# Kernel tuning notes

Measured on AMD Instinct MI355X. Metric: run time of the kernel, lower is better.

## Reference

```python
import jax, jax.numpy as jnp
import numpy as np

B, S, E, H = 2, 2048, 1024, 16
D = E // H  # head_dim = 64
FE = 4      # forward_expansion
EPS = 1e-5


def layernorm(x, g, b):
    mu = jnp.mean(x, axis=-1, keepdims=True)
    var = jnp.var(x, axis=-1, keepdims=True)
    return (x - mu) * jax.lax.rsqrt(var + EPS) * g + b


def setup_inputs() -> dict:
    key = jax.random.key(0)
    ks = jax.random.split(key, 16)
    s = lambda d: 1.0 / np.sqrt(d)
    return {
        "queries": jax.random.normal(ks[0], (B, S, E), jnp.float32),
        "keys": jax.random.normal(ks[1], (B, S, E), jnp.float32),
        "values": jax.random.normal(ks[2], (B, S, E), jnp.float32),
        "mask": jnp.ones((B, 1, S, S), jnp.int32),  # ignored (faithful to source bug)
        "Wq": jax.random.normal(ks[3], (D, D), jnp.float32) * s(D),
        "Wk": jax.random.normal(ks[4], (D, D), jnp.float32) * s(D),
        "Wv": jax.random.normal(ks[5], (D, D), jnp.float32) * s(D),
        "Wfc": jax.random.normal(ks[6], (E, E), jnp.float32) * s(E),
        "bfc": jnp.zeros((E,), jnp.float32),
        "W1": jax.random.normal(ks[7], (FE * E, E), jnp.float32) * s(E),
        "b1": jnp.zeros((FE * E,), jnp.float32),
        "W2": jax.random.normal(ks[8], (E, FE * E), jnp.float32) * s(FE * E),
        "b2": jnp.zeros((E,), jnp.float32),
        "ln1_g": jnp.ones((E,), jnp.float32),
        "ln1_b": jnp.zeros((E,), jnp.float32),
        "ln2_g": jnp.ones((E,), jnp.float32),
        "ln2_b": jnp.zeros((E,), jnp.float32),
    }


def reference(queries, keys, values, mask, Wq, Wk, Wv, Wfc, bfc, W1, b1, W2, b2,
              ln1_g, ln1_b, ln2_g, ln2_b):
    # --- MHA ---
    q = queries.reshape(B, S, H, D) @ Wq.T  # [B,S,H,D]
    k = keys.reshape(B, S, H, D) @ Wk.T
    v = values.reshape(B, S, H, D) @ Wv.T
    scores = jnp.einsum('bqhd,bkhd->bhqk', q, k)
    # source: softmax(scores / S**(-1/2)) == scores * sqrt(S)  (faithful quirk)
    # mask is ignored: source masked_fill is non-inplace and discarded
    attn = jax.nn.softmax(scores * jnp.sqrt(jnp.float32(S)), axis=-1)
    out = jnp.einsum('bhqk,bkhd->bqhd', attn, v).reshape(B, S, E)
    att = out @ Wfc.T + bfc
    # --- residual + LN + FFN + LN (dropout p=0 -> identity) ---
    h = layernorm(att + queries, ln1_g, ln1_b)
    x = jax.nn.relu(h @ W1.T + b1) @ W2.T + b2
    return layernorm(x + h, ln2_g, ln2_b)
```

## Files before the change

### kernel.cpp

```cpp
#include <hip/hip_runtime.h>
#include <hip/hip_bf16.h>
#include <math.h>

#define B_ 2
#define S_ 2048
#define E_ 1024
#define H_ 16
#define D_ 64
#define TOK (B_*S_)
#define SCALE2 (45.254833995939045f * 1.44269504088896340f)

typedef __bf16 bf16x8 __attribute__((ext_vector_type(8)));
typedef float floatx4 __attribute__((ext_vector_type(4)));
struct b4s { __hip_bfloat16 x, y, z, w; };

typedef const __attribute__((address_space(1))) char ga_char;
typedef __attribute__((address_space(3))) char ls_char;

__device__ __forceinline__ void gload_lds16(const void* g, ls_char* l) {
  __builtin_amdgcn_global_load_lds((ga_char*)g, l, 16, 0, 0);
}

#if __has_builtin(__builtin_amdgcn_exp2f)
#define EXP2(x) __builtin_amdgcn_exp2f(x)
#else
#define EXP2(x) exp2f(x)
#endif

#define SWZ(arr, half, row, qpos) \
  (*(bf16x8*)&arr[half][row][(((qpos) ^ ((row) & 3)) * 8)])

__device__ __forceinline__ void sbar() {
  asm volatile("" ::: "memory");
  __builtin_amdgcn_s_barrier();
  asm volatile("" ::: "memory");
}

__global__ __launch_bounds__(256) void cast_all(
    const float* __restrict__ Wfc, const float* __restrict__ W1,
    const float* __restrict__ W2, __hip_bfloat16* __restrict__ Wfcb,
    __hip_bfloat16* __restrict__ W1b, __hip_bfloat16* __restrict__ W2b,
    const float* __restrict__ Wq, const float* __restrict__ Wk,
    const float* __restrict__ Wv, __hip_bfloat16* __restrict__ Whl) {
  const int i = blockIdx.x * 256 + threadIdx.x;
  if (i < 2359296) {
    const float* src; __hip_bfloat16* dst; int j;
    if (i < 262144)       { src = Wfc; dst = Wfcb; j = i; }
    else if (i < 1310720) { src = W1;  dst = W1b;  j = i - 262144; }
    else                  { src = W2;  dst = W2b;  j = i - 1310720; }
    float4 v = ((const float4*)src)[j];
    b4s o;
    o.x = __float2bfloat16(v.x); o.y = __float2bfloat16(v.y);
    o.z = __float2bfloat16(v.z); o.w = __float2bfloat16(v.w);
    *(b4s*)(dst + (size_t)j * 4) = o;
  } else if (i < 2362368) {
    const int idx = i - 2359296;
    const int m = idx >> 10;
    const int off = (idx & 1023) * 4;
    const float* W = (m == 0) ? Wq : (m == 1) ? Wk : Wv;
    float4 v = *(const float4*)(W + off);
    b4s hi, lo;
    hi.x = __float2bfloat16(v.x); lo.x = __float2bfloat16(v.x - __bfloat162float(hi.x));
    hi.y = __float2bfloat16(v.y); lo.y = __float2bfloat16(v.y - __bfloat162float(hi.y));
    hi.z = __float2bfloat16(v.z); lo.z = __float2bfloat16(v.z - __bfloat162float(hi.z));
    hi.w = __float2bfloat16(v.w); lo.w = __float2bfloat16(v.w - __bfloat162float(hi.w));
    *(b4s*)(Whl + (size_t)m * 8192 + off) = hi;
    *(b4s*)(Whl + (size_t)m * 8192 + 4096 + off) = lo;
  }
}

__global__ __launch_bounds__(256) void qkv_fused(
    const float* __restrict__ xq, const float* __restrict__ xk,
    const float* __restrict__ xv, const __hip_bfloat16* __restrict__ Whl,
    __hip_bfloat16* __restrict__ qhi, __hip_bfloat16* __restrict__ qlo,
    __hip_bfloat16* __restrict__ khi, __hip_bfloat16* __restrict__ klo,
    __hip_bfloat16* __restrict__ vt) {
  __shared__ __bf16 Xh[2][64][32], Xl[2][64][32];
  __shared__ __bf16 Vt[64][72];
  const int t = threadIdx.x, lane = t & 63, w = t >> 6;
  const int quad = lane >> 4, low = lane & 15;
  const int bh = blockIdx.y;
  const int b = bh >> 4, h = bh & 15;
  const int s0 = blockIdx.x * 64;
  const int sr = t >> 2;
  const int sc = (t & 3) * 16;
  const int scc = sc >> 5;
  const int p0 = (sc & 31) >> 3;

  for (int m = 0; m < 3; m++) {
    const float* xin = (m == 0) ? xq : (m == 1) ? xk : xv;
    const __hip_bfloat16* Wh = Whl + (size_t)m * 8192;
    const float sc_m = (m == 0) ? SCALE2 : 1.0f;

    __syncthreads();
    {
      const float* src = xin + ((size_t)(b * S_ + s0 + sr)) * E_ + h * 64 + sc;
      float4 f0 = *(const float4*)(src);
      float4 f1 = *(const float4*)(src + 4);
      float4 f2 = *(const float4*)(src + 8);
      float4 f3 = *(const float4*)(src + 12);
      float fv[16] = {f0.x, f0.y, f0.z, f0.w, f1.x, f1.y, f1.z, f1.w,
                      f2.x, f2.y, f2.z, f2.w, f3.x, f3.y, f3.z, f3.w};
      bf16x8 hi0, hi1, lo0, lo1;
      #pragma unroll
      for (int j = 0; j < 8; j++) {
        hi0[j] = (__bf16)fv[j];
        lo0[j] = (__bf16)(fv[j] - (float)hi0[j]);
        hi1[j] = (__bf16)fv[8 + j];
        lo1[j] = (__bf16)(fv[8 + j] - (float)hi1[j]);
      }
      SWZ(Xh, scc, sr, p0) = hi0;
      SWZ(Xh, scc, sr, p0 + 1) = hi1;
      SWZ(Xl, scc, sr, p0) = lo0;
      SWZ(Xl, scc, sr, p0 + 1) = lo1;
    }
    __syncthreads();

    bf16x8 ah[2], al[2];
    #pragma unroll
    for (int c = 0; c < 2; c++) {
      ah[c] = SWZ(Xh, c, w * 16 + low, quad);
      al[c] = SWZ(Xl, c, w * 16 + low, quad);
    }

    floatx4 acc[4];
    #pragma unroll
    for (int nn = 0; nn < 4; nn++) {
      floatx4 a = {};
      #pragma unroll
      for (int c = 0; c < 2; c++) {
        const __hip_bfloat16* wp = Wh + (nn * 16 + low) * 64 + c * 32 + quad * 8;
        bf16x8 wh_ = *(const bf16x8*)wp;
        bf16x8 wl_ = *(const bf16x8*)(wp + 4096);
        a = __builtin_amdgcn_mfma_f32_16x16x32_bf16(ah[c], wh_, a, 0, 0, 0);
        a = __builtin_amdgcn_mfma_f32_16x16x32_bf16(al[c], wh_, a, 0, 0, 0);
        a = __builtin_amdgcn_mfma_f32_16x16x32_bf16(ah[c], wl_, a, 0, 0, 0);
      }
      acc[nn] = a;
    }

    if (m < 2) {
      __hip_bfloat16* dh = (m == 0) ? qhi : khi;
      __hip_bfloat16* dl = (m == 0) ? qlo : klo;
      #pragma unroll
      for (int nn = 0; nn < 4; nn++) {
        #pragma unroll
        for (int i = 0; i < 4; i++) {
          const int s = s0 + w * 16 + quad * 4 + i;
          const int d = nn * 16 + low;
          const size_t adr = ((size_t)bh * S_ + s) * 64 + d;
          const float f = acc[nn][i] * sc_m;
          const __hip_bfloat16 hb = __float2bfloat16(f);
          dh[adr] = hb;
          dl[adr] = __float2bfloat16(f - __bfloat162float(hb));
        }
      }
    } else {
      #pragma unroll
      for (int nn = 0; nn < 4; nn++)
        #pragma unroll
        for (int i = 0; i < 4; i++)
          Vt[nn * 16 + low][w * 16 + quad * 4 + i] = (__bf16)acc[nn][i];
      __syncthreads();
      const int dr = t >> 2;
      const int scl = (t & 3) * 16;
      __hip_bfloat16* dst = vt + ((size_t)bh * 64 + dr) * S_ + s0 + scl;
      bf16x8 o0 = *(const bf16x8*)&Vt[dr][scl];
      bf16x8 o1 = *(const bf16x8*)&Vt[dr][scl + 8];
      *(bf16x8*)dst = o0;
      *(bf16x8*)(dst + 8) = o1;
    }
  }
}

__device__ __forceinline__ void softmax_update(
    const floatx4* sa, floatx4* oacc, float& mrow, float& lrow, bf16x8* pb) {
  float rmax;
  {
    float m0 = fmaxf(fmaxf(sa[0][0], sa[0][1]), fmaxf(sa[0][2], sa[0][3]));
    float m1 = fmaxf(fmaxf(sa[1][0], sa[1][1]), fmaxf(sa[1][2], sa[1][3]));
    float m2 = fmaxf(fmaxf(sa[2][0], sa[2][1]), fmaxf(sa[2][2], sa[2][3]));
    float m3 = fmaxf(fmaxf(sa[3][0], sa[3][1]), fmaxf(sa[3][2], sa[3][3]));
    rmax = fmaxf(fmaxf(m0, m1), fmaxf(m2, m3));
    rmax = fmaxf(rmax, __shfl_xor(rmax, 16, 64));
    rmax = fmaxf(rmax, __shfl_xor(rmax, 32, 64));
  }
  if (__any(rmax > mrow)) {
    const float nm = fmaxf(mrow, rmax);
    const float al = EXP2(mrow - nm);
    mrow = nm;
    lrow *= al;
    #pragma unroll
    for (int dt = 0; dt < 4; dt++) {
      oacc[dt][0] *= al; oacc[dt][1] *= al;
      oacc[dt][2] *= al; oacc[dt][3] *= al;
    }
  }
  float p[4][4];
  float rs;
  {
    float r0_ = 0.f, r1_ = 0.f, r2_ = 0.f, r3_ = 0.f;
    #pragma unroll
    for (int i = 0; i < 4; i++) {
      p[0][i] = EXP2(sa[0][i] - mrow); r0_ += p[0][i];
      p[1][i] = EXP2(sa[1][i] - mrow); r1_ += p[1][i];
      p[2][i] = EXP2(sa[2][i] - mrow); r2_ += p[2][i];
      p[3][i] = EXP2(sa[3][i] - mrow); r3_ += p[3][i];
    }
    rs = (r0_ + r1_) + (r2_ + r3_);
    rs += __shfl_xor(rs, 16, 64);
    rs += __shfl_xor(rs, 32, 64);
  }
  lrow += rs;
  #pragma unroll
  for (int kh2 = 0; kh2 < 2; kh2++) {
    bf16x8 v;
    v[0] = (__bf16)p[kh2][0]; v[1] = (__bf16)p[kh2][1];
    v[2] = (__bf16)p[kh2][2]; v[3] = (__bf16)p[kh2][3];
    v[4] = (__bf16)p[kh2 + 2][0]; v[5] = (__bf16)p[kh2 + 2][1];
    v[6] = (__bf16)p[kh2 + 2][2]; v[7] = (__bf16)p[kh2 + 2][3];
    pb[kh2] = v;
  }
}

__global__ __launch_bounds__(512, 4) void attn_mfma(
    const __hip_bfloat16* __restrict__ Qhi, const __hip_bfloat16* __restrict__ Qlo,
    const __hip_bfloat16* __restrict__ Khi, const __hip_bfloat16* __restrict__ Klo,
    const __hip_bfloat16* __restrict__ Vtg, __hip_bfloat16* __restrict__ ctx) {
  __shared__ __bf16 Kh[2][2][64][32], Kl[2][2][64][32], Vs[2][2][64][32];
  const int t = threadIdx.x, lane = t & 63, w = t >> 6;
  const int quad = lane >> 4, low = lane & 15;
  const int bh = blockIdx.x;
  const int qw = blockIdx.y * 128 + w * 16;

  const int sh = w >> 2;
  const int r0 = (w & 3) * 16;
  const int srow = r0 + (lane >> 2);
  const int sq = (lane & 3) ^ (srow & 3);
  const __hip_bfloat16* gK = Khi + ((size_t)bh * S_ + srow) * 64 + sh * 32 + sq * 8;
  const __hip_bfloat16* gL = Klo + ((size_t)bh * S_ + srow) * 64 + sh * 32 + sq * 8;
  const __hip_bfloat16* gV = Vtg + ((size_t)bh * 64 + srow) * S_ + sh * 32 + sq * 8;

  bf16x8 qh[2], ql[2];
  {
    const size_t qbase = ((size_t)bh * S_ + qw + low) * 64 + quad * 8;
    qh[0] = *(const bf16x8*)(Qhi + qbase);
    qh[1] = *(const bf16x8*)(Qhi + qbase + 32);
    ql[0] = *(const bf16x8*)(Qlo + qbase);
    ql[1] = *(const bf16x8*)(Qlo + qbase + 32);
  }

  floatx4 oacc[4] = {};
  float mrow = -3e38f, lrow = 0.f;

  gload_lds16(gK, (ls_char*)&Kh[0][sh][r0][0]);
  gload_lds16(gL, (ls_char*)&Kl[0][sh][r0][0]);
  gload_lds16(gV, (ls_char*)&Vs[0][sh][r0][0]);

  for (int kt = 0; kt < S_ / 64; kt++) {
    const int cur = kt & 1;
    __syncthreads();
    if (kt + 1 < S_ / 64) {
      gload_lds16(gK + (size_t)(kt + 1) * 4096, (ls_char*)&Kh[cur ^ 1][sh][r0][0]);
      gload_lds16(gL + (size_t)(kt + 1) * 4096, (ls_char*)&Kl[cur ^ 1][sh][r0][0]);
      gload_lds16(gV + (size_t)(kt + 1) * 64,   (ls_char*)&Vs[cur ^ 1][sh][r0][0]);
    }

    floatx4 sa[4];
    __builtin_amdgcn_s_setprio(1);
    #pragma unroll
    for (int nn = 0; nn < 4; nn++) {
      const int prow = (nn & 1) * 32 + (nn >> 1) * 4 + (low >> 2) * 8 + (low & 3);
      bf16x8 kh0 = SWZ(Kh[cur], 0, prow, quad);
      bf16x8 kh1 = SWZ(Kh[cur], 1, prow, quad);
      bf16x8 kl0 = SWZ(Kl[cur], 0, prow, quad);
      bf16x8 kl1 = SWZ(Kl[cur], 1, prow, quad);
      floatx4 s = {};
      s = __builtin_amdgcn_mfma_f32_16x16x32_bf16(kh0, qh[0], s, 0, 0, 0);
      s = __builtin_amdgcn_mfma_f32_16x16x32_bf16(kh1, qh[1], s, 0, 0, 0);
      s = __builtin_amdgcn_mfma_f32_16x16x32_bf16(kl0, qh[0], s, 0, 0, 0);
      s = __builtin_amdgcn_mfma_f32_16x16x32_bf16(kl1, qh[1], s, 0, 0, 0);
      s = __builtin_amdgcn_mfma_f32_16x16x32_bf16(kh0, ql[0], s, 0, 0, 0);
      s = __builtin_amdgcn_mfma_f32_16x16x32_bf16(kh1, ql[1], s, 0, 0, 0);
      sa[nn] = s;
    }
    __builtin_amdgcn_s_setprio(0);

    bf16x8 pb[2];
    softmax_update(sa, oacc, mrow, lrow, pb);

    __builtin_amdgcn_s_setprio(1);
    #pragma unroll
    for (int dt = 0; dt < 4; dt++) {
      bf16x8 vb0 = SWZ(Vs[cur], 0, dt * 16 + low, quad);
      bf16x8 vb1 = SWZ(Vs[cur], 1, dt * 16 + low, quad);
      oacc[dt] = __builtin_amdgcn_mfma_f32_16x16x32_bf16(vb0, pb[0], oacc[dt], 0, 0, 0);
      oacc[dt] = __builtin_amdgcn_mfma_f32_16x16x32_bf16(vb1, pb[1], oacc[dt], 0, 0, 0);
    }
    __builtin_amdgcn_s_setprio(0);
  }

  const float inv = 1.0f / lrow;
  const int b = bh >> 4, h = bh & 15;
  const size_t base = ((size_t)(b * S_ + qw + low)) * E_ + h * 64 + quad * 4;
  #pragma unroll
  for (int dt = 0; dt < 4; dt++) {
    b4s o;
    o.x = __float2bfloat16(oacc[dt][0] * inv);
    o.y = __float2bfloat16(oacc[dt][1] * inv);
    o.z = __float2bfloat16(oacc[dt][2] * inv);
    o.w = __float2bfloat16(oacc[dt][3] * inv);
    *(b4s*)(ctx + base + dt * 16) = o;
  }
}

template <int RELU, int OUT_BF16, int PARTIAL>
__global__ __launch_bounds__(256) void gemm_mfma(
    const __hip_bfloat16* __restrict__ A, const __hip_bfloat16* __restrict__ Wt,
    const float* __restrict__ bias, void* __restrict__ C0, void* __restrict__ C1,
    int M, int N, int Kblk, int lda) {
  __shared__ __bf16 As[2][128][64];
  __shared__ __bf16 Bs[2][128][64];
  const int t = threadIdx.x;
  const int lane = t & 63;
  const int w = t >> 6;
  const int wr = w >> 1, wc = w & 1;
  const int m0 = blockIdx.y * 128, n0 = blockIdx.x * 128;
  void* Cout = (blockIdx.z == 0) ? C0 : C1;

  A += (size_t)blockIdx.z * Kblk;
  Wt += (size_t)blockIdx.z * Kblk;

  floatx4 acc[4][4] = {};
  const int srow = t >> 3;
  const int ssc = ((t & 7) ^ (srow & 7)) * 8;

  const __hip_bfloat16* gA = A + (size_t)(m0 + srow) * lda + ssc;
  const __hip_bfloat16* gB = Wt + (size_t)(n0 + srow) * lda + ssc;
  const size_t rstep = (size_t)32 * lda;

#define GSTAGE(buf, k0) do {                                      \
    ls_char* lA = (ls_char*)&As[buf][0][0] + w * 1024;            \
    ls_char* lB = (ls_char*)&Bs[buf][0][0] + w * 1024;            \
    gload_lds16(gA + (k0),             lA);                       \
    gload_lds16(gA + (k0) + rstep,     lA + 4096);                \
    gload_lds16(gA + (k0) + 2 * rstep, lA + 8192);                \
    gload_lds16(gA + (k0) + 3 * rstep, lA + 12288);               \
    gload_lds16(gB + (k0),             lB);                       \
    gload_lds16(gB + (k0) + rstep,     lB + 4096);                \
    gload_lds16(gB + (k0) + 2 * rstep, lB + 8192);                \
    gload_lds16(gB + (k0) + 3 * rstep, lB + 12288);               \
  } while (0)

  GSTAGE(0, 0);
  const int nsteps = Kblk >> 6;
  for (int st = 0; st < nsteps; st++) {
    const int cur = st & 1;
    __syncthreads();
    if (st + 1 < nsteps) GSTAGE(cur ^ 1, (st + 1) * 64);

    #pragma unroll
    for (int ks = 0; ks < 2; ks++) {
      bf16x8 af[4], bfr[4];
      #pragma unroll
      for (int i = 0; i < 4; i++) {
        const int ra = wr * 64 + i * 16 + (lane & 15);
        const int ca = (((lane >> 4) + ks * 4) ^ (ra & 7)) * 8;
        af[i] = *(const bf16x8*)&As[cur][ra][ca];
        const int rb = wc * 64 + i * 16 + (lane & 15);
        const int cb = (((lane >> 4) + ks * 4) ^ (rb & 7)) * 8;
        bfr[i] = *(const bf16x8*)&Bs[cur][rb][cb];
      }
      #pragma unroll
      for (int mi = 0; mi < 4; mi++)
        #pragma unroll
        for (int ni = 0; ni < 4; ni++)
          acc[mi][ni] = __builtin_amdgcn_mfma_f32_16x16x32_bf16(
              af[mi], bfr[ni], acc[mi][ni], 0, 0, 0);
    }
  }
#undef GSTAGE

  const int cil = lane & 15;
  const int quad = lane >> 4;
  #pragma unroll
  for (int ni = 0; ni < 4; ni++) {
    const int col = n0 + wc * 64 + ni * 16 + cil;
    const float bb = PARTIAL ? 0.f : bias[col];
    #pragma unroll
    for (int mi = 0; mi < 4; mi++) {
      const int row = m0 + wr * 64 + mi * 16 + quad * 4;
      #pragma unroll
      for (int i = 0; i < 4; i++) {
        if (PARTIAL) {
          ((float*)Cout)[(size_t)(row + i) * N + col] = acc[mi][ni][i];
        } else {
          float vv = acc[mi][ni][i] + bb;
          if (RELU) vv = fmaxf(vv, 0.f);
          if (OUT_BF16)
            ((__hip_bfloat16*)Cout)[(size_t)(row + i) * N + col] = __float2bfloat16(vv);
          else
            ((float*)Cout)[(size_t)(row + i) * N + col] = vv;
        }
      }
    }
  }
}

__global__ __launch_bounds__(512, 2) void gemm_ff1(
    const __hip_bfloat16* __restrict__ A, const __hip_bfloat16* __restrict__ Wt,
    const float* __restrict__ bias, __hip_bfloat16* __restrict__ C) {
  __shared__ __bf16 As[2][256][64];
  __shared__ __bf16 Bs[2][256][64];
  const int t = threadIdx.x, lane = t & 63, w = t >> 6;
  const int quad = lane >> 4, low = lane & 15;
  const int wm = w >> 2, wn = w & 3;
  const int m0 = blockIdx.y * 256, n0 = blockIdx.x * 256;

  floatx4 acc[8][4] = {};

  const int srow = t >> 3;
  const int ssc = ((t & 7) ^ (srow & 7)) * 8;
  const __hip_bfloat16* gA = A + (size_t)(m0 + srow) * 1024 + ssc;
  const __hip_bfloat16* gB = Wt + (size_t)(n0 + srow) * 1024 + ssc;

#define FSTAGE(buf, k0) do {                                        \
    ls_char* lA = (ls_char*)&As[buf][0][0] + w * 1024;              \
    ls_char* lB = (ls_char*)&Bs[buf][0][0] + w * 1024;              \
    gload_lds16(gA + (k0),          lA);                            \
    gload_lds16(gA + (k0) + 65536,  lA + 8192);                     \
    gload_lds16(gA + (k0) + 131072, lA + 16384);                    \
    gload_lds16(gA + (k0) + 196608, lA + 24576);                    \
    gload_lds16(gB + (k0),          lB);                            \
    gload_lds16(gB + (k0) + 65536,  lB + 8192);                     \
    gload_lds16(gB + (k0) + 131072, lB + 16384);                    \
    gload_lds16(gB + (k0) + 196608, lB + 24576);                    \
  } while (0)

#define LDA_HALF(mh) do {                                                     \
    _Pragma("unroll")                                                         \
    for (int mi = 0; mi < 4; mi++) {                                          \
      const int ra = wm * 128 + (mh) * 64 + mi * 16 + low;                    \
      af[mi][0] = *(const bf16x8*)&As[cur][ra][((quad) ^ (ra & 7)) * 8];      \
      af[mi][1] = *(const bf16x8*)&As[cur][ra][((4 + quad) ^ (ra & 7)) * 8];  \
    }                                                                         \
  } while (0)

#define LDB_HALF(dst, nh) do {                                                \
    _Pragma("unroll")                                                         \
    for (int ni = 0; ni < 2; ni++) {                                          \
      const int rb = wn * 64 + (nh) * 32 + ni * 16 + low;                     \
      dst[ni][0] = *(const bf16x8*)&Bs[cur][rb][((quad) ^ (rb & 7)) * 8];     \
      dst[ni][1] = *(const bf16x8*)&Bs[cur][rb][((4 + quad) ^ (rb & 7)) * 8]; \
    }                                                                         \
  } while (0)

#define MFMA_Q(bfr, mh, nh) do {                                              \
    __builtin_amdgcn_s_setprio(1);                                            \
    _Pragma("unroll")                                                         \
    for (int mi = 0; mi < 4; mi++)                                            \
      _Pragma("unroll")                                                       \
      for (int ni = 0; ni < 2; ni++) {                                        \
        acc[(mh)*4+mi][(nh)*2+ni] = __builtin_amdgcn_mfma_f32_16x16x32_bf16(  \
            af[mi][0], bfr[ni][0], acc[(mh)*4+mi][(nh)*2+ni], 0, 0, 0);       \
        acc[(mh)*4+mi][(nh)*2+ni] = __builtin_amdgcn_mfma_f32_16x16x32_bf16(  \
            af[mi][1], bfr[ni][1], acc[(mh)*4+mi][(nh)*2+ni], 0, 0, 0);       \
      }                                                                       \
    __builtin_amdgcn_s_setprio(0);                                            \
  } while (0)

  FSTAGE(0, 0);
  bf16x8 af[4][2], bA[2][2], bB[2][2];

  for (int kt = 0; kt < 16; kt++) {
    const int cur = kt & 1;
    __syncthreads();

    LDA_HALF(0);
    LDB_HALF(bA, 0);
    sbar();
    MFMA_Q(bA, 0, 0);
    sbar();

    LDB_HALF(bB, 1);
    if (kt + 1 < 16) FSTAGE(cur ^ 1, (kt + 1) * 64);
    sbar();
    MFMA_Q(bB, 0, 1);
    sbar();

    LDA_HALF(1);
    sbar();
    MFMA_Q(bB, 1, 1);
    sbar();

    MFMA_Q(bA, 1, 0);
  }
#undef FSTAGE
#undef LDA_HALF
#undef LDB_HALF
#undef MFMA_Q

  #pragma unroll
  for (int ni = 0; ni < 4; ni++) {
    const int col = n0 + wn * 64 + ni * 16 + low;
    const float bb = bias[col];
    #pragma unroll
    for (int mi = 0; mi < 8; mi++) {
      const int row = m0 + wm * 128 + mi * 16 + quad * 4;
      #pragma unroll
      for (int i = 0; i < 4; i++) {
        float vv = fmaxf(acc[mi][ni][i] + bb, 0.f);
        C[(size_t)(row + i) * 4096 + col] = __float2bfloat16(vv);
      }
    }
  }
}

template <int EMIT_BF16, int HAS_A1, int HAS_BIAS>
__global__ __launch_bounds__(256) void add_ln(
    const float* __restrict__ a0, const float* __restrict__ a1,
    const float* __restrict__ r, const float* __restrict__ bias,
    const float* __restrict__ g, const float* __restrict__ bt,
    float* __restrict__ out, __hip_bfloat16* __restrict__ outb) {
  __shared__ float red[16];
  const int tok = blockIdx.x, t = threadIdx.x;
  float4 av = ((const float4*)(a0 + (size_t)tok * E_))[t];
  float4 rv = ((const float4*)(r + (size_t)tok * E_))[t];
  float4 x;
  x.x = av.x + rv.x; x.y = av.y + rv.y; x.z = av.z + rv.z; x.w = av.w + rv.w;
  if (HAS_A1) {
    float4 a2 = ((const float4*)(a1 + (size_t)tok * E_))[t];
    x.x += a2.x; x.y += a2.y; x.z += a2.z; x.w += a2.w;
  }
  if (HAS_BIAS) {
    float4 cv = ((const float4*)bias)[t];
    x.x += cv.x; x.y += cv.y; x.z += cv.z; x.w += cv.w;
  }
  float sum = x.x + x.y + x.z + x.w;
  float ssq = x.x * x.x + x.y * x.y + x.z * x.z + x.w * x.w;
  #pragma unroll
  for (int off = 32; off >= 1; off >>= 1) {
    sum += __shfl_down(sum, off, 64);
    ssq += __shfl_down(ssq, off, 64);
  }
  const int wave = t >> 6;
  if ((t & 63) == 0) { red[wave] = sum; red[4 + wave] = ssq; }
  __syncthreads();
  if (t == 0) {
    float s = red[0] + red[1] + red[2] + red[3];
    float qq = red[4] + red[5] + red[6] + red[7];
    float mu = s * (1.0f / E_);
    red[8] = mu;
    red[9] = qq * (1.0f / E_) - mu * mu;
  }
  __syncthreads();
  const float mu = red[8];
  const float inv = rsqrtf(red[9] + 1e-5f);
  float4 gv = ((const float4*)g)[t];
  float4 bv = ((const float4*)bt)[t];
  float4 o;
  o.x = (x.x - mu) * inv * gv.x + bv.x;
  o.y = (x.y - mu) * inv * gv.y + bv.y;
  o.z = (x.z - mu) * inv * gv.z + bv.z;
  o.w = (x.w - mu) * inv * gv.w + bv.w;
  ((float4*)(out + (size_t)tok * E_))[t] = o;
  if (EMIT_BF16) {
    b4s ob;
    ob.x = __float2bfloat16(o.x); ob.y = __float2bfloat16(o.y);
    ob.z = __float2bfloat16(o.z); ob.w = __float2bfloat16(o.w);
    *(b4s*)(outb + (size_t)tok * E_ + t * 4) = ob;
  }
}

extern "C" void kernel_launch(void* const* d_in, const int* in_sizes, int n_in,
                              void* d_out, int out_size, void* d_ws, size_t ws_size,
                              hipStream_t stream) {
  const float* queries = (const float*)d_in[0];
  const float* keys    = (const float*)d_in[1];
  const float* values  = (const float*)d_in[2];
  const float* Wq  = (const float*)d_in[4];
  const float* Wk  = (const float*)d_in[5];
  const float* Wv  = (const float*)d_in[6];
  const float* Wfc = (const float*)d_in[7];
  const float* bfc = (const float*)d_in[8];
  const float* W1  = (const float*)d_in[9];
  const float* b1  = (const float*)d_in[10];
  const float* W2  = (const float*)d_in[11];
  const float* b2  = (const float*)d_in[12];
  const float* ln1_g = (const float*)d_in[13];
  const float* ln1_b = (const float*)d_in[14];
  const float* ln2_g = (const float*)d_in[15];
  const float* ln2_b = (const float*)d_in[16];

  const size_t M1 = 1048576;
  float* ws = (float*)d_ws;
  float* P0  = ws;
  float* P1  = ws + 4 * M1;
  float* Hf  = ws + 8 * M1;
  __hip_bfloat16* bb = (__hip_bfloat16*)(ws + 12 * M1);
  __hip_bfloat16* CTXb = bb;
  __hip_bfloat16* Hb   = bb + 4 * M1;
  __hip_bfloat16* Wfcb = bb + 8 * M1;
  __hip_bfloat16* W1b  = bb + 9 * M1;
  __hip_bfloat16* W2b  = bb + 13 * M1;
  __hip_bfloat16* Qhi  = bb + 17 * M1;
  __hip_bfloat16* Qlo  = bb + 21 * M1;
  __hip_bfloat16* Khi  = bb + 25 * M1;
  __hip_bfloat16* Klo  = bb + 29 * M1;
  __hip_bfloat16* Vtb  = bb + 33 * M1;
  __hip_bfloat16* FF1b = bb + 17 * M1;
  __hip_bfloat16* Whlb = bb + 37 * M1;
  float* out = (float*)d_out;

  cast_all<<<9228, 256, 0, stream>>>(Wfc, W1, W2, Wfcb, W1b, W2b,
                                     Wq, Wk, Wv, Whlb);

  qkv_fused<<<dim3(S_ / 64, B_ * H_), 256, 0, stream>>>(
      queries, keys, values, Whlb, Qhi, Qlo, Khi, Klo, Vtb);
  attn_mfma<<<dim3(B_ * H_, S_ / 128), 512, 0, stream>>>(
      Qhi, Qlo, Khi, Klo, Vtb, CTXb);
  gemm_mfma<0, 0, 1><<<dim3(E_ / 128, TOK / 128, 2), 256, 0, stream>>>(
      CTXb, Wfcb, nullptr, P0, P1, TOK, E_, 512, E_);
  add_ln<1, 1, 1><<<TOK, 256, 0, stream>>>(
      P0, P1, queries, bfc, ln1_g, ln1_b, Hf, Hb);
  gemm_ff1<<<dim3(4 * E_ / 256, TOK / 256), 512, 0, stream>>>(
      Hb, W1b, b1, FF1b);
  gemm_mfma<0, 0, 1><<<dim3(E_ / 128, TOK / 128, 2), 256, 0, stream>>>(
      FF1b, W2b, nullptr, P0, P1, TOK, E_, 2048, 4 * E_);
  add_ln<0, 1, 1><<<TOK, 256, 0, stream>>>(
      P0, P1, Hf, b2, ln2_g, ln2_b, out, nullptr);
}
```

Baseline: 389.0 us.

## Interleave split global-to-LDS prefetch with MFMA phases in FF1 GEMM

```diff
diff --git a/kernel.cpp b/kernel.cpp
--- a/kernel.cpp
+++ b/kernel.cpp
@@ -35,6 +35,7 @@
   __builtin_amdgcn_s_barrier();
   asm volatile("" ::: "memory");
 }
+#define VMW(n) asm volatile("s_waitcnt vmcnt(" #n ")" ::: "memory")
 
 __global__ __launch_bounds__(256) void cast_all(
     const float* __restrict__ Wfc, const float* __restrict__ W1,
@@ -424,17 +425,23 @@
   const __hip_bfloat16* gA = A + (size_t)(m0 + srow) * 1024 + ssc;
   const __hip_bfloat16* gB = Wt + (size_t)(n0 + srow) * 1024 + ssc;
 
-#define FSTAGE(buf, k0) do {                                        \
-    ls_char* lA = (ls_char*)&As[buf][0][0] + w * 1024;              \
-    ls_char* lB = (ls_char*)&Bs[buf][0][0] + w * 1024;              \
-    gload_lds16(gA + (k0),          lA);                            \
-    gload_lds16(gA + (k0) + 65536,  lA + 8192);                     \
-    gload_lds16(gA + (k0) + 131072, lA + 16384);                    \
-    gload_lds16(gA + (k0) + 196608, lA + 24576);                    \
-    gload_lds16(gB + (k0),          lB);                            \
-    gload_lds16(gB + (k0) + 65536,  lB + 8192);                     \
-    gload_lds16(gB + (k0) + 131072, lB + 16384);                    \
-    gload_lds16(gB + (k0) + 196608, lB + 24576);                    \
+#define LA(buf) ((ls_char*)&As[buf][0][0] + w * 1024)
+#define LB(buf) ((ls_char*)&Bs[buf][0][0] + w * 1024)
+#define ST_A0(buf, k0) do {                                   \
+    gload_lds16(gA + (k0),          LA(buf));                 \
+    gload_lds16(gA + (k0) + 131072, LA(buf) + 16384);         \
+  } while (0)
+#define ST_A1(buf, k0) do {                                   \
+    gload_lds16(gA + (k0) + 65536,  LA(buf) + 8192);          \
+    gload_lds16(gA + (k0) + 196608, LA(buf) + 24576);         \
+  } while (0)
+#define ST_B0(buf, k0) do {                                   \
+    gload_lds16(gB + (k0),          LB(buf));                 \
+    gload_lds16(gB + (k0) + 65536,  LB(buf) + 8192);          \
+  } while (0)
+#define ST_B1(buf, k0) do {                                   \
+    gload_lds16(gB + (k0) + 131072, LB(buf) + 16384);         \
+    gload_lds16(gB + (k0) + 196608, LB(buf) + 24576);         \
   } while (0)
 
 #define LDA_HALF(mh) do {                                                     \
@@ -449,7 +456,7 @@
 #define LDB_HALF(dst, nh) do {                                                \
     _Pragma("unroll")                                                         \
     for (int ni = 0; ni < 2; ni++) {                                          \
-      const int rb = wn * 64 + (nh) * 32 + ni * 16 + low;                     \
+      const int rb = (nh) * 128 + wn * 32 + ni * 16 + low;                    \
       dst[ni][0] = *(const bf16x8*)&Bs[cur][rb][((quad) ^ (rb & 7)) * 8];     \
       dst[ni][1] = *(const bf16x8*)&Bs[cur][rb][((4 + quad) ^ (rb & 7)) * 8]; \
     }                                                                         \
@@ -469,47 +476,59 @@
     __builtin_amdgcn_s_setprio(0);                                            \
   } while (0)
 
-  FSTAGE(0, 0);
+  ST_A0(0, 0); ST_B0(0, 0); ST_B1(0, 0); ST_A1(0, 0);
+
   bf16x8 af[4][2], bA[2][2], bB[2][2];
 
   for (int kt = 0; kt < 16; kt++) {
-    const int cur = kt & 1;
-    __syncthreads();
-
+    const int cur = kt & 1, nxt = cur ^ 1;
+    const int kn = (kt + 1) * 64;
+    const bool more = (kt + 1 < 16);
+
+    VMW(4);
+    sbar();
     LDA_HALF(0);
     LDB_HALF(bA, 0);
+    if (more) ST_A0(nxt, kn);
+    MFMA_Q(bA, 0, 0);
+
+    if (kt < 15) { VMW(4); } else { VMW(2); }
     sbar();
-    MFMA_Q(bA, 0, 0);
+    LDB_HALF(bB, 1);
+    if (more) ST_B0(nxt, kn);
+    MFMA_Q(bB, 0, 1);
+
+    if (kt < 15) { VMW(4); } else { VMW(0); }
     sbar();
-
-    LDB_HALF(bB, 1);
-    if (kt + 1 < 16) FSTAGE(cur ^ 1, (kt + 1) * 64);
+    LDA_HALF(1);
+    if (more) ST_B1(nxt, kn);
+    MFMA_Q(bB, 1, 1);
+
     sbar();
-    MFMA_Q(bB, 0, 1);
-    sbar();
-
-    LDA_HALF(1);
-    sbar();
-    MFMA_Q(bB, 1, 1);
-    sbar();
-
+    if (more) ST_A1(nxt, kn);
     MFMA_Q(bA, 1, 0);
   }
-#undef FSTAGE
+#undef ST_A0
+#undef ST_A1
+#undef ST_B0
+#undef ST_B1
+#undef LA
+#undef LB
 #undef LDA_HALF
 #undef LDB_HALF
 #undef MFMA_Q
 
   #pragma unroll
-  for (int ni = 0; ni < 4; ni++) {
-    const int col = n0 + wn * 64 + ni * 16 + low;
+  for (int n4 = 0; n4 < 4; n4++) {
+    const int nh = n4 >> 1, ni = n4 & 1;
+    const int col = n0 + nh * 128 + wn * 32 + ni * 16 + low;
     const float bb = bias[col];
     #pragma unroll
     for (int mi = 0; mi < 8; mi++) {
       const int row = m0 + wm * 128 + mi * 16 + quad * 4;
       #pragma unroll
       for (int i = 0; i < 4; i++) {
-        float vv = fmaxf(acc[mi][ni][i] + bb, 0.f);
+        float vv = fmaxf(acc[mi][n4][i] + bb, 0.f);
         C[(size_t)(row + i) * 4096 + col] = __float2bfloat16(vv);
       }
     }
```

New measurement: 377.2 us. 1.03x faster.
